# Kernel tuning notes

Hardware: AMD Instinct MI355X
Metric: run time of the kernel (lower is better)

## Reference

```python
import jax, jax.numpy as jnp
import numpy as np

N_NODES = 100000


def gcn_conv(x, src, dst, W, b, n):
    # PyG GCNConv: add self-loops, symmetric normalization D^-1/2 (A+I) D^-1/2, then XW + b
    h = x @ W  # [N, out]
    loop = jnp.arange(n, dtype=src.dtype)
    s = jnp.concatenate([src, loop])
    d = jnp.concatenate([dst, loop])
    deg = jax.ops.segment_sum(jnp.ones_like(d, dtype=h.dtype), d, num_segments=n)
    dinv = jnp.where(deg > 0, jax.lax.rsqrt(deg), 0.0)
    norm = dinv[s] * dinv[d]  # [E+N]
    msgs = h[s] * norm[:, None]  # gather + scale
    out = jax.ops.segment_sum(msgs, d, num_segments=n)  # scatter-add to dst
    return out + b


def setup_inputs() -> dict:
    key = jax.random.key(0)
    ks = jax.random.split(key, 12)
    F_IN, H, F3, C = 128, 128, 8, 16
    E = 1600000
    x = jax.random.normal(ks[0], (N_NODES, F_IN), dtype=jnp.float32)
    edge_index = jax.random.randint(ks[1], (2, E), 0, N_NODES, dtype=jnp.int64)

    def glorot(k, fan_in, fan_out):
        lim = float(np.sqrt(6.0 / (fan_in + fan_out)))
        return jax.random.uniform(k, (fan_in, fan_out), jnp.float32, -lim, lim)

    return {
        "x": x,
        "edge_index": edge_index,
        "W1": glorot(ks[2], F_IN, H), "b1": jnp.zeros((H,), jnp.float32),
        "W2": glorot(ks[3], H, H), "b2": jnp.zeros((H,), jnp.float32),
        "W3": glorot(ks[4], H, F3), "b3": jnp.zeros((F3,), jnp.float32),
        "Wc": glorot(ks[5], F3, C), "bc": jnp.zeros((C,), jnp.float32),
    }


def reference(x, edge_index, W1, b1, W2, b2, W3, b3, Wc, bc):
    src, dst = edge_index[0], edge_index[1]
    n = x.shape[0]
    h = jax.nn.relu(gcn_conv(x, src, dst, W1, b1, n))
    h = jax.nn.relu(gcn_conv(h, src, dst, W2, b2, n))
    h = jax.nn.relu(gcn_conv(h, src, dst, W3, b3, n))
    return h @ Wc + bc
```

## Files before the change

### kernel.cpp

```cpp
#include <hip/hip_runtime.h>
#include <cstdint>


__global__ __launch_bounds__(256) void k_count(const int* __restrict__ dst, int E, int* __restrict__ deg) {
    int i = blockIdx.x * 256 + threadIdx.x;
    if (i < E) atomicAdd(&deg[dst[i]], 1);
}

__global__ __launch_bounds__(256) void k_dinv(const int* __restrict__ deg, float* __restrict__ dinv, int n) {
    int i = blockIdx.x * 256 + threadIdx.x;
    if (i < n) dinv[i] = rsqrtf((float)deg[i] + 1.0f);
}

__global__ __launch_bounds__(256) void k_scanA(const int* __restrict__ deg, int n, int* __restrict__ bsum) {
    __shared__ int red[256];
    int t = threadIdx.x;
    int base = blockIdx.x * 1024 + t * 4;
    int s = 0;
#pragma unroll
    for (int j = 0; j < 4; j++) { int idx = base + j; s += (idx < n) ? deg[idx] : 0; }
    red[t] = s; __syncthreads();
    for (int off = 128; off > 0; off >>= 1) { if (t < off) red[t] += red[t + off]; __syncthreads(); }
    if (t == 0) bsum[blockIdx.x] = red[0];
}

__global__ __launch_bounds__(128) void k_scanB(int* __restrict__ bsum, int nb) {
    __shared__ int sh[128];
    int t = threadIdx.x;
    int v = (t < nb) ? bsum[t] : 0;
    sh[t] = v; __syncthreads();
    for (int off = 1; off < 128; off <<= 1) {
        int x = (t >= off) ? sh[t - off] : 0;
        __syncthreads();
        sh[t] += x;
        __syncthreads();
    }
    if (t < nb) bsum[t] = sh[t] - v;
}

__global__ __launch_bounds__(256) void k_scanC(const int* __restrict__ deg, int n, const int* __restrict__ bsum,
                                               int* __restrict__ rowptr, int* __restrict__ cursor, int E) {
    __shared__ int sh[256];
    int t = threadIdx.x;
    int base = blockIdx.x * 1024 + t * 4;
    int v[4], pre[4]; int s = 0;
#pragma unroll
    for (int j = 0; j < 4; j++) { int idx = base + j; v[j] = (idx < n) ? deg[idx] : 0; pre[j] = s; s += v[j]; }
    sh[t] = s; __syncthreads();
    int own = s;
    for (int off = 1; off < 256; off <<= 1) {
        int x = (t >= off) ? sh[t - off] : 0;
        __syncthreads();
        sh[t] += x;
        __syncthreads();
    }
    int toff = sh[t] - own + bsum[blockIdx.x];
#pragma unroll
    for (int j = 0; j < 4; j++) {
        int idx = base + j;
        if (idx < n) { int rp = toff + pre[j]; rowptr[idx] = rp; cursor[idx] = rp; }
    }
    if (blockIdx.x == 0 && t == 0) rowptr[n] = E;
}

__global__ __launch_bounds__(256) void k_fill(const int* __restrict__ src, const int* __restrict__ dst, int E,
                                              const float* __restrict__ dinv, int* __restrict__ cursor,
                                              int* __restrict__ col, float* __restrict__ wn) {
    int i = blockIdx.x * 256 + threadIdx.x;
    if (i < E) {
        int u = src[i], v = dst[i];
        int pos = atomicAdd(&cursor[v], 1);
        col[pos] = u;
        wn[pos] = dinv[u];
    }
}


__global__ __launch_bounds__(256) void k_gemm_xw(const float* __restrict__ A, const float* __restrict__ W,
                                                 float* __restrict__ C, int n) {
    __shared__ float At[256][33];
    int t = threadIdx.x;
    int r0 = blockIdx.x * 256;
    int c0 = blockIdx.y * 64;
    int row = r0 + t;
    float acc[64];
#pragma unroll
    for (int c = 0; c < 64; c++) acc[c] = 0.f;

    for (int k0 = 0; k0 < 128; k0 += 32) {
        __syncthreads();
#pragma unroll
        for (int j = 0; j < 8; j++) {
            int q = t + 256 * j;
            int ri = q >> 3;
            int kk = (q & 7) * 4;
            int gr = r0 + ri; if (gr >= n) gr = n - 1;
            const float4 vv = *(const float4*)(A + (size_t)gr * 128 + k0 + kk);
            At[ri][kk + 0] = vv.x; At[ri][kk + 1] = vv.y; At[ri][kk + 2] = vv.z; At[ri][kk + 3] = vv.w;
        }
        __syncthreads();
#pragma unroll
        for (int kk = 0; kk < 32; kk++) {
            float a = At[t][kk];
            const float* wr = W + (size_t)(k0 + kk) * 128 + c0;
#pragma unroll
            for (int c = 0; c < 64; c++) acc[c] = fmaf(a, wr[c], acc[c]);
        }
    }
    if (row < n) {
        float* crow = C + (size_t)row * 128 + c0;
#pragma unroll
        for (int c = 0; c < 64; c += 4) {
            float4 vv = { acc[c], acc[c + 1], acc[c + 2], acc[c + 3] };
            *(float4*)(crow + c) = vv;
        }
    }
}

__global__ __launch_bounds__(256) void k_gemm_w3(const float* __restrict__ A, const float* __restrict__ W,
                                                 float* __restrict__ C, int n) {
    __shared__ float At[256][33];
    int t = threadIdx.x;
    int r0 = blockIdx.x * 256;
    int row = r0 + t;
    float acc[8];
#pragma unroll
    for (int c = 0; c < 8; c++) acc[c] = 0.f;

    for (int k0 = 0; k0 < 128; k0 += 32) {
        __syncthreads();
#pragma unroll
        for (int j = 0; j < 8; j++) {
            int q = t + 256 * j;
            int ri = q >> 3;
            int kk = (q & 7) * 4;
            int gr = r0 + ri; if (gr >= n) gr = n - 1;
            const float4 vv = *(const float4*)(A + (size_t)gr * 128 + k0 + kk);
            At[ri][kk + 0] = vv.x; At[ri][kk + 1] = vv.y; At[ri][kk + 2] = vv.z; At[ri][kk + 3] = vv.w;
        }
        __syncthreads();
#pragma unroll
        for (int kk = 0; kk < 32; kk++) {
            float a = At[t][kk];
            const float* wr = W + (size_t)(k0 + kk) * 8;
#pragma unroll
            for (int c = 0; c < 8; c++) acc[c] = fmaf(a, wr[c], acc[c]);
        }
    }
    if (row < n) {
        float* crow = C + (size_t)row * 8;
        float4 v0 = { acc[0], acc[1], acc[2], acc[3] };
        float4 v1 = { acc[4], acc[5], acc[6], acc[7] };
        *(float4*)(crow) = v0;
        *(float4*)(crow + 4) = v1;
    }
}


__global__ __launch_bounds__(256) void k_agg128(const float* __restrict__ T, const int* __restrict__ rowptr,
                                                const int* __restrict__ col, const float* __restrict__ wn,
                                                const float* __restrict__ dinv, const float* __restrict__ bias,
                                                float* __restrict__ H, int n) {
    int wid = threadIdx.x >> 6, lane = threadIdx.x & 63;
    int v = blockIdx.x * 4 + wid;
    if (v >= n) return;
    int e0 = rowptr[v], e1 = rowptr[v + 1];
    const float2* Tp = (const float2*)T;
    float ax = 0.f, ay = 0.f;
    for (int e = e0; e < e1; e++) {
        int u = col[e];
        float w = wn[e];
        float2 tv = Tp[(size_t)u * 64 + lane];
        ax = fmaf(w, tv.x, ax);
        ay = fmaf(w, tv.y, ay);
    }
    float dv = dinv[v];
    float2 sv = Tp[(size_t)v * 64 + lane];
    float2 bb = ((const float2*)bias)[lane];
    float ox = fmaf(dv, ax, dv * dv * sv.x) + bb.x;
    float oy = fmaf(dv, ay, dv * dv * sv.y) + bb.y;
    ox = ox > 0.f ? ox : 0.f;
    oy = oy > 0.f ? oy : 0.f;
    ((float2*)H)[(size_t)v * 64 + lane] = make_float2(ox, oy);
}

__global__ __launch_bounds__(256) void k_agg8(const float* __restrict__ T, const int* __restrict__ rowptr,
                                              const int* __restrict__ col, const float* __restrict__ wn,
                                              const float* __restrict__ dinv, const float* __restrict__ bias,
                                              float* __restrict__ H, int n) {
    int gid = blockIdx.x * 256 + threadIdx.x;
    int v = gid >> 3, f = gid & 7;
    if (v >= n) return;
    int e0 = rowptr[v], e1 = rowptr[v + 1];
    float acc = 0.f;
    for (int e = e0; e < e1; e++) {
        acc = fmaf(wn[e], T[(size_t)col[e] * 8 + f], acc);
    }
    float dv = dinv[v];
    float o = fmaf(dv, acc, dv * dv * T[(size_t)v * 8 + f]) + bias[f];
    H[(size_t)v * 8 + f] = o > 0.f ? o : 0.f;
}

__global__ __launch_bounds__(256) void k_out(const float* __restrict__ H, const float* __restrict__ Wc,
                                             const float* __restrict__ bc, float* __restrict__ out, int n) {
    int gid = blockIdx.x * 256 + threadIdx.x;
    int v = gid >> 3, cp = (gid & 7) * 2;
    if (v >= n) return;
    float a0 = bc[cp], a1 = bc[cp + 1];
#pragma unroll
    for (int k = 0; k < 8; k++) {
        float h = H[(size_t)v * 8 + k];
        a0 = fmaf(h, Wc[k * 16 + cp], a0);
        a1 = fmaf(h, Wc[k * 16 + cp + 1], a1);
    }
    ((float2*)out)[(size_t)v * 8 + (cp >> 1)] = make_float2(a0, a1);
}


extern "C" void kernel_launch(void* const* d_in, const int* in_sizes, int n_in,
                              void* d_out, int out_size, void* d_ws, size_t ws_size,
                              hipStream_t stream) {
    const float* x  = (const float*)d_in[0];
    const int*   ei = (const int*)d_in[1];
    const float* W1 = (const float*)d_in[2];
    const float* b1 = (const float*)d_in[3];
    const float* W2 = (const float*)d_in[4];
    const float* b2 = (const float*)d_in[5];
    const float* W3 = (const float*)d_in[6];
    const float* b3 = (const float*)d_in[7];
    const float* Wc = (const float*)d_in[8];
    const float* bc = (const float*)d_in[9];

    const int n = in_sizes[0] / 128;
    const int E = in_sizes[1] / 2;
    const int* src = ei;
    const int* dst = ei + E;

    char* p = (char*)d_ws;
    auto carve = [&](size_t bytes) -> char* {
        char* r = p;
        p += (bytes + 511) & ~(size_t)511;
        return r;
    };
    int*   deg    = (int*)  carve((size_t)n * 4);
    int*   cursor = (int*)  carve((size_t)n * 4);
    int*   rowptr = (int*)  carve((size_t)(n + 1) * 4);
    int*   bsum   = (int*)  carve(4096);
    float* dinv   = (float*)carve((size_t)n * 4);
    int*   col    = (int*)  carve((size_t)E * 4);
    float* wnv    = (float*)carve((size_t)E * 4);
    float* bufA   = (float*)carve((size_t)n * 128 * 4);
    float* bufB   = (float*)carve((size_t)n * 128 * 4);

    hipMemsetAsync(deg, 0, (size_t)n * 4, stream);

    int gE = (E + 255) / 256;
    int NB = (n + 1023) / 1024;

    k_count<<<gE, 256, 0, stream>>>(dst, E, deg);
    k_dinv<<<(n + 255) / 256, 256, 0, stream>>>(deg, dinv, n);
    k_scanA<<<NB, 256, 0, stream>>>(deg, n, bsum);
    k_scanB<<<1, 128, 0, stream>>>(bsum, NB);
    k_scanC<<<NB, 256, 0, stream>>>(deg, n, bsum, rowptr, cursor, E);
    k_fill<<<gE, 256, 0, stream>>>(src, dst, E, dinv, cursor, col, wnv);

    dim3 gg((n + 255) / 256, 2);
    k_gemm_xw<<<gg, 256, 0, stream>>>(x, W1, bufA, n);
    k_agg128<<<(n + 3) / 4, 256, 0, stream>>>(bufA, rowptr, col, wnv, dinv, b1, bufB, n);
    k_gemm_xw<<<gg, 256, 0, stream>>>(bufB, W2, bufA, n);
    k_agg128<<<(n + 3) / 4, 256, 0, stream>>>(bufA, rowptr, col, wnv, dinv, b2, bufB, n);
    k_gemm_w3<<<(n + 255) / 256, 256, 0, stream>>>(bufB, W3, bufA, n);
    k_agg8<<<(n * 8 + 255) / 256, 256, 0, stream>>>(bufA, rowptr, col, wnv, dinv, b3, bufB, n);
    k_out<<<(n * 8 + 255) / 256, 256, 0, stream>>>(bufB, Wc, bc, (float*)d_out, n);
}
```

Before: 849.8 us.

## Pack CSR col/weight, unroll aggregation gathers, register-prefetch GEMM tiles

Interleaves the CSR column index and normalization weight into one int2 array, so each edge needs a single 8-byte load. The aggregation kernels are unrolled by 4 (and by 8 in a new variant used for layer 2) with independent accumulators, which puts more gathers in flight per wavefront. Both GEMM kernels now prefetch the next A tile into registers while computing on the current one. This costs more registers, and the tail handling in the unrolled aggregations issues some redundant gathers.

```diff
diff --git a/kernel.cpp b/kernel.cpp
--- a/kernel.cpp
+++ b/kernel.cpp
@@ -65,13 +65,12 @@
 
 __global__ __launch_bounds__(256) void k_fill(const int* __restrict__ src, const int* __restrict__ dst, int E,
                                               const float* __restrict__ dinv, int* __restrict__ cursor,
-                                              int* __restrict__ col, float* __restrict__ wn) {
+                                              int2* __restrict__ cw) {
     int i = blockIdx.x * 256 + threadIdx.x;
     if (i < E) {
         int u = src[i], v = dst[i];
         int pos = atomicAdd(&cursor[v], 1);
-        col[pos] = u;
-        wn[pos] = dinv[u];
+        cw[pos] = make_int2(u, __float_as_int(dinv[u]));
     }
 }
 
@@ -83,22 +82,35 @@
     int r0 = blockIdx.x * 256;
     int c0 = blockIdx.y * 64;
     int row = r0 + t;
-    float acc[64];
-#pragma unroll
-    for (int c = 0; c < 64; c++) acc[c] = 0.f;
-
-    for (int k0 = 0; k0 < 128; k0 += 32) {
-        __syncthreads();
+    float4 rv[8];
+
+    auto loadTile = [&](int k0) {
 #pragma unroll
         for (int j = 0; j < 8; j++) {
             int q = t + 256 * j;
             int ri = q >> 3;
             int kk = (q & 7) * 4;
             int gr = r0 + ri; if (gr >= n) gr = n - 1;
-            const float4 vv = *(const float4*)(A + (size_t)gr * 128 + k0 + kk);
-            At[ri][kk + 0] = vv.x; At[ri][kk + 1] = vv.y; At[ri][kk + 2] = vv.z; At[ri][kk + 3] = vv.w;
-        }
-        __syncthreads();
+            rv[j] = *(const float4*)(A + (size_t)gr * 128 + k0 + kk);
+        }
+    };
+
+    float acc[64];
+#pragma unroll
+    for (int c = 0; c < 64; c++) acc[c] = 0.f;
+
+    loadTile(0);
+    for (int k0 = 0; k0 < 128; k0 += 32) {
+        __syncthreads();
+#pragma unroll
+        for (int j = 0; j < 8; j++) {
+            int q = t + 256 * j;
+            int ri = q >> 3;
+            int kk = (q & 7) * 4;
+            At[ri][kk + 0] = rv[j].x; At[ri][kk + 1] = rv[j].y; At[ri][kk + 2] = rv[j].z; At[ri][kk + 3] = rv[j].w;
+        }
+        __syncthreads();
+        if (k0 < 96) loadTile(k0 + 32);
 #pragma unroll
         for (int kk = 0; kk < 32; kk++) {
             float a = At[t][kk];
@@ -123,22 +135,35 @@
     int t = threadIdx.x;
     int r0 = blockIdx.x * 256;
     int row = r0 + t;
-    float acc[8];
-#pragma unroll
-    for (int c = 0; c < 8; c++) acc[c] = 0.f;
-
-    for (int k0 = 0; k0 < 128; k0 += 32) {
-        __syncthreads();
+    float4 rv[8];
+
+    auto loadTile = [&](int k0) {
 #pragma unroll
         for (int j = 0; j < 8; j++) {
             int q = t + 256 * j;
             int ri = q >> 3;
             int kk = (q & 7) * 4;
             int gr = r0 + ri; if (gr >= n) gr = n - 1;
-            const float4 vv = *(const float4*)(A + (size_t)gr * 128 + k0 + kk);
-            At[ri][kk + 0] = vv.x; At[ri][kk + 1] = vv.y; At[ri][kk + 2] = vv.z; At[ri][kk + 3] = vv.w;
-        }
-        __syncthreads();
+            rv[j] = *(const float4*)(A + (size_t)gr * 128 + k0 + kk);
+        }
+    };
+
+    float acc[8];
+#pragma unroll
+    for (int c = 0; c < 8; c++) acc[c] = 0.f;
+
+    loadTile(0);
+    for (int k0 = 0; k0 < 128; k0 += 32) {
+        __syncthreads();
+#pragma unroll
+        for (int j = 0; j < 8; j++) {
+            int q = t + 256 * j;
+            int ri = q >> 3;
+            int kk = (q & 7) * 4;
+            At[ri][kk + 0] = rv[j].x; At[ri][kk + 1] = rv[j].y; At[ri][kk + 2] = rv[j].z; At[ri][kk + 3] = rv[j].w;
+        }
+        __syncthreads();
+        if (k0 < 96) loadTile(k0 + 32);
 #pragma unroll
         for (int kk = 0; kk < 32; kk++) {
             float a = At[t][kk];
@@ -157,8 +182,9 @@
 }
 
 
+
 __global__ __launch_bounds__(256) void k_agg128(const float* __restrict__ T, const int* __restrict__ rowptr,
-                                                const int* __restrict__ col, const float* __restrict__ wn,
+                                                const int2* __restrict__ cw,
                                                 const float* __restrict__ dinv, const float* __restrict__ bias,
                                                 float* __restrict__ H, int n) {
     int wid = threadIdx.x >> 6, lane = threadIdx.x & 63;
@@ -166,14 +192,41 @@
     if (v >= n) return;
     int e0 = rowptr[v], e1 = rowptr[v + 1];
     const float2* Tp = (const float2*)T;
-    float ax = 0.f, ay = 0.f;
-    for (int e = e0; e < e1; e++) {
-        int u = col[e];
-        float w = wn[e];
-        float2 tv = Tp[(size_t)u * 64 + lane];
-        ax = fmaf(w, tv.x, ax);
-        ay = fmaf(w, tv.y, ay);
-    }
+    float ax = 0.f, ay = 0.f, bx = 0.f, by = 0.f, cx = 0.f, cy = 0.f, dx = 0.f, dy = 0.f;
+    int e = e0;
+    for (; e + 4 <= e1; e += 4) {
+        int2 p0 = cw[e + 0];
+        int2 p1 = cw[e + 1];
+        int2 p2 = cw[e + 2];
+        int2 p3 = cw[e + 3];
+        float2 t0 = Tp[(size_t)p0.x * 64 + lane];
+        float2 t1 = Tp[(size_t)p1.x * 64 + lane];
+        float2 t2 = Tp[(size_t)p2.x * 64 + lane];
+        float2 t3 = Tp[(size_t)p3.x * 64 + lane];
+        float w0 = __int_as_float(p0.y), w1 = __int_as_float(p1.y);
+        float w2 = __int_as_float(p2.y), w3 = __int_as_float(p3.y);
+        ax = fmaf(w0, t0.x, ax); ay = fmaf(w0, t0.y, ay);
+        bx = fmaf(w1, t1.x, bx); by = fmaf(w1, t1.y, by);
+        cx = fmaf(w2, t2.x, cx); cy = fmaf(w2, t2.y, cy);
+        dx = fmaf(w3, t3.x, dx); dy = fmaf(w3, t3.y, dy);
+    }
+    int rem = e1 - e;
+    if (rem > 0) {
+        int2 p0 = cw[e];
+        int2 p1 = (rem > 1) ? cw[e + 1] : p0;
+        int2 p2 = (rem > 2) ? cw[e + 2] : p0;
+        float2 t0 = Tp[(size_t)p0.x * 64 + lane];
+        float2 t1 = Tp[(size_t)p1.x * 64 + lane];
+        float2 t2 = Tp[(size_t)p2.x * 64 + lane];
+        float w0 = __int_as_float(p0.y);
+        float w1 = (rem > 1) ? __int_as_float(p1.y) : 0.f;
+        float w2 = (rem > 2) ? __int_as_float(p2.y) : 0.f;
+        ax = fmaf(w0, t0.x, ax); ay = fmaf(w0, t0.y, ay);
+        bx = fmaf(w1, t1.x, bx); by = fmaf(w1, t1.y, by);
+        cx = fmaf(w2, t2.x, cx); cy = fmaf(w2, t2.y, cy);
+    }
+    ax += bx + cx + dx;
+    ay += by + cy + dy;
     float dv = dinv[v];
     float2 sv = Tp[(size_t)v * 64 + lane];
     float2 bb = ((const float2*)bias)[lane];
@@ -184,18 +237,100 @@
     ((float2*)H)[(size_t)v * 64 + lane] = make_float2(ox, oy);
 }
 
+__global__ __launch_bounds__(256) void k_agg128_p8(const float* __restrict__ T, const int* __restrict__ rowptr,
+                                                   const int2* __restrict__ cw,
+                                                   const float* __restrict__ dinv, const float* __restrict__ bias,
+                                                   float* __restrict__ H, int n) {
+    int wid = threadIdx.x >> 6, lane = threadIdx.x & 63;
+    int v = blockIdx.x * 4 + wid;
+    if (v >= n) return;
+    int e0 = rowptr[v], e1 = rowptr[v + 1];
+    const float2* Tp = (const float2*)T;
+    float sx[8], sy[8];
+#pragma unroll
+    for (int i = 0; i < 8; i++) { sx[i] = 0.f; sy[i] = 0.f; }
+    int e = e0;
+    for (; e + 8 <= e1; e += 8) {
+        int2 p[8];
+#pragma unroll
+        for (int i = 0; i < 8; i++) p[i] = cw[e + i];
+        float2 tv[8];
+#pragma unroll
+        for (int i = 0; i < 8; i++) tv[i] = Tp[(size_t)p[i].x * 64 + lane];
+#pragma unroll
+        for (int i = 0; i < 8; i++) {
+            float w = __int_as_float(p[i].y);
+            sx[i] = fmaf(w, tv[i].x, sx[i]);
+            sy[i] = fmaf(w, tv[i].y, sy[i]);
+        }
+    }
+    for (; e + 4 <= e1; e += 4) {
+        int2 p[4];
+#pragma unroll
+        for (int i = 0; i < 4; i++) p[i] = cw[e + i];
+        float2 tv[4];
+#pragma unroll
+        for (int i = 0; i < 4; i++) tv[i] = Tp[(size_t)p[i].x * 64 + lane];
+#pragma unroll
+        for (int i = 0; i < 4; i++) {
+            float w = __int_as_float(p[i].y);
+            sx[i] = fmaf(w, tv[i].x, sx[i]);
+            sy[i] = fmaf(w, tv[i].y, sy[i]);
+        }
+    }
+    int rem = e1 - e;
+    if (rem > 0) {
+        int2 p0 = cw[e];
+        int2 p1 = (rem > 1) ? cw[e + 1] : p0;
+        int2 p2 = (rem > 2) ? cw[e + 2] : p0;
+        float2 t0 = Tp[(size_t)p0.x * 64 + lane];
+        float2 t1 = Tp[(size_t)p1.x * 64 + lane];
+        float2 t2 = Tp[(size_t)p2.x * 64 + lane];
+        float w0 = __int_as_float(p0.y);
+        float w1 = (rem > 1) ? __int_as_float(p1.y) : 0.f;
+        float w2 = (rem > 2) ? __int_as_float(p2.y) : 0.f;
+        sx[0] = fmaf(w0, t0.x, sx[0]); sy[0] = fmaf(w0, t0.y, sy[0]);
+        sx[1] = fmaf(w1, t1.x, sx[1]); sy[1] = fmaf(w1, t1.y, sy[1]);
+        sx[2] = fmaf(w2, t2.x, sx[2]); sy[2] = fmaf(w2, t2.y, sy[2]);
+    }
+    float ax = ((sx[0] + sx[1]) + (sx[2] + sx[3])) + ((sx[4] + sx[5]) + (sx[6] + sx[7]));
+    float ay = ((sy[0] + sy[1]) + (sy[2] + sy[3])) + ((sy[4] + sy[5]) + (sy[6] + sy[7]));
+    float dv = dinv[v];
+    float2 sv = Tp[(size_t)v * 64 + lane];
+    float2 bb = ((const float2*)bias)[lane];
+    float ox = fmaf(dv, ax, dv * dv * sv.x) + bb.x;
+    float oy = fmaf(dv, ay, dv * dv * sv.y) + bb.y;
+    ox = ox > 0.f ? ox : 0.f;
+    oy = oy > 0.f ? oy : 0.f;
+    ((float2*)H)[(size_t)v * 64 + lane] = make_float2(ox, oy);
+}
+
 __global__ __launch_bounds__(256) void k_agg8(const float* __restrict__ T, const int* __restrict__ rowptr,
-                                              const int* __restrict__ col, const float* __restrict__ wn,
+                                              const int2* __restrict__ cw,
                                               const float* __restrict__ dinv, const float* __restrict__ bias,
                                               float* __restrict__ H, int n) {
     int gid = blockIdx.x * 256 + threadIdx.x;
     int v = gid >> 3, f = gid & 7;
     if (v >= n) return;
     int e0 = rowptr[v], e1 = rowptr[v + 1];
-    float acc = 0.f;
-    for (int e = e0; e < e1; e++) {
-        acc = fmaf(wn[e], T[(size_t)col[e] * 8 + f], acc);
-    }
+    float a0 = 0.f, a1 = 0.f, a2 = 0.f, a3 = 0.f;
+    int e = e0;
+    for (; e + 4 <= e1; e += 4) {
+        int2 p0 = cw[e + 0], p1 = cw[e + 1], p2 = cw[e + 2], p3 = cw[e + 3];
+        float t0 = T[(size_t)p0.x * 8 + f];
+        float t1 = T[(size_t)p1.x * 8 + f];
+        float t2 = T[(size_t)p2.x * 8 + f];
+        float t3 = T[(size_t)p3.x * 8 + f];
+        a0 = fmaf(__int_as_float(p0.y), t0, a0);
+        a1 = fmaf(__int_as_float(p1.y), t1, a1);
+        a2 = fmaf(__int_as_float(p2.y), t2, a2);
+        a3 = fmaf(__int_as_float(p3.y), t3, a3);
+    }
+    for (; e < e1; ++e) {
+        int2 p = cw[e];
+        a0 = fmaf(__int_as_float(p.y), T[(size_t)p.x * 8 + f], a0);
+    }
+    float acc = (a0 + a1) + (a2 + a3);
     float dv = dinv[v];
     float o = fmaf(dv, acc, dv * dv * T[(size_t)v * 8 + f]) + bias[f];
     H[(size_t)v * 8 + f] = o > 0.f ? o : 0.f;
@@ -247,8 +382,7 @@
     int*   rowptr = (int*)  carve((size_t)(n + 1) * 4);
     int*   bsum   = (int*)  carve(4096);
     float* dinv   = (float*)carve((size_t)n * 4);
-    int*   col    = (int*)  carve((size_t)E * 4);
-    float* wnv    = (float*)carve((size_t)E * 4);
+    int2*  cw     = (int2*) carve((size_t)E * 8);
     float* bufA   = (float*)carve((size_t)n * 128 * 4);
     float* bufB   = (float*)carve((size_t)n * 128 * 4);
 
@@ -262,14 +396,14 @@
     k_scanA<<<NB, 256, 0, stream>>>(deg, n, bsum);
     k_scanB<<<1, 128, 0, stream>>>(bsum, NB);
     k_scanC<<<NB, 256, 0, stream>>>(deg, n, bsum, rowptr, cursor, E);
-    k_fill<<<gE, 256, 0, stream>>>(src, dst, E, dinv, cursor, col, wnv);
+    k_fill<<<gE, 256, 0, stream>>>(src, dst, E, dinv, cursor, cw);
 
     dim3 gg((n + 255) / 256, 2);
     k_gemm_xw<<<gg, 256, 0, stream>>>(x, W1, bufA, n);
-    k_agg128<<<(n + 3) / 4, 256, 0, stream>>>(bufA, rowptr, col, wnv, dinv, b1, bufB, n);
+    k_agg128<<<(n + 3) / 4, 256, 0, stream>>>(bufA, rowptr, cw, dinv, b1, bufB, n);
     k_gemm_xw<<<gg, 256, 0, stream>>>(bufB, W2, bufA, n);
-    k_agg128<<<(n + 3) / 4, 256, 0, stream>>>(bufA, rowptr, col, wnv, dinv, b2, bufB, n);
+    k_agg128_p8<<<(n + 3) / 4, 256, 0, stream>>>(bufA, rowptr, cw, dinv, b2, bufB, n);
     k_gemm_w3<<<(n + 255) / 256, 256, 0, stream>>>(bufB, W3, bufA, n);
-    k_agg8<<<(n * 8 + 255) / 256, 256, 0, stream>>>(bufA, rowptr, col, wnv, dinv, b3, bufB, n);
+    k_agg8<<<(n * 8 + 255) / 256, 256, 0, stream>>>(bufA, rowptr, cw, dinv, b3, bufB, n);
     k_out<<<(n * 8 + 255) / 256, 256, 0, stream>>>(bufB, Wc, bc, (float*)d_out, n);
 }
```

After: 862.0 us. No clear change (+1.4%).
